# Optimization experiments

Hardware: AMD Instinct MI355X
Metric: run time of the kernel (lower is better)

## Reference

```python
import jax, jax.numpy as jnp
import numpy as np

B, S, H, E, I, MAX_K, A_HID = 2, 2048, 1024, 8, 2688, 6, 50


def setup_inputs() -> dict:
    key = jax.random.key(0)
    ks = jax.random.split(key, 10)
    sc = 0.02
    return {
        "hidden_states": jax.random.normal(ks[0], (B, S, H), dtype=jnp.float32),
        "router_w": jax.random.normal(ks[1], (E, H), dtype=jnp.float32) * sc,
        "actor_w1": jax.random.normal(ks[2], (A_HID, H), dtype=jnp.float32) * sc,
        "actor_b1": jnp.zeros((A_HID,), dtype=jnp.float32),
        "actor_w2": jax.random.normal(ks[3], (MAX_K, A_HID), dtype=jnp.float32) * sc,
        "actor_b2": jnp.zeros((MAX_K,), dtype=jnp.float32),
        "gate_w": jax.random.normal(ks[4], (E, I, H), dtype=jnp.float32) * sc,
        "up_w": jax.random.normal(ks[5], (E, I, H), dtype=jnp.float32) * sc,
        "down_w": jax.random.normal(ks[6], (E, H, I), dtype=jnp.float32) * sc,
    }


def reference(hidden_states, router_w, actor_w1, actor_b1, actor_w2, actor_b2,
              gate_w, up_w, down_w):
    # Router: frozen linear -> softmax probs  [B,S,E]
    probs = jax.nn.softmax(
        jnp.einsum("bsh,eh->bse", hidden_states, router_w).astype(jnp.float32),
        axis=-1)

    # Allocator (ActorCritic.actor): Linear -> GELU -> Linear, clamp(-30,30)
    a_h = jax.nn.gelu(jnp.einsum("bsh,ah->bsa", hidden_states, actor_w1) + actor_b1)
    actor_logits = jnp.clip(
        jnp.einsum("bsa,ka->bsk", a_h, actor_w2) + actor_b2, -30.0, 30.0)
    # deterministic per-token k in [1, MAX_K]
    sampled_k = jnp.argmax(actor_logits, axis=-1) + 1  # [B,S] int

    # dynamic_topk_indices_and_scores: iterative argmax+scatter == select the
    # k highest-prob experts per token; keep their scores, zero elsewhere.
    order = jnp.argsort(-probs, axis=-1)           # descending order of experts
    rank = jnp.argsort(order, axis=-1)             # rank[e] = position of expert e
    mask = rank < sampled_k[..., None]             # [B,S,E] bool, top-k selected
    scores = jnp.where(mask, probs, 0.0).astype(hidden_states.dtype)

    # Expert dispatch-combine: out = sum_e scores[...,e] * LlamaMLP_e(x)
    out = jnp.zeros_like(hidden_states)
    for e in range(E):  # fixed small loop over experts
        g = jnp.einsum("bsh,ih->bsi", hidden_states, gate_w[e])
        u = jnp.einsum("bsh,ih->bsi", hidden_states, up_w[e])
        y = jnp.einsum("bsi,hi->bsh", jax.nn.silu(g) * u, down_w[e])
        out = out + scores[..., e:e + 1] * y
    return out
```

## Files before the change

kernel.cpp:

```cpp
#include <hip/hip_runtime.h>
#include <hip/hip_bf16.h>
#include <stdint.h>

#define TOK 4096
#define HD  1024
#define NE  8
#define ID  2688
#define MAXK 6
#define AHID 50
#define NROW 58
#define KCH 64
#define NCH (HD / KCH)

#define BM 128
#define BN 128
#define BK 64
#define NTM (TOK / BM)
#define NID2 (2 * ID)
#define NTN_GUC (NID2 / BN)
#define NB_GUC (NTN_GUC * NTM)
#define NTN_D (HD / BN)
#define NB_D (NTN_D * NTM)

typedef float  f32x4  __attribute__((ext_vector_type(4)));
typedef __bf16 bf16x8 __attribute__((ext_vector_type(8)));
typedef ushort ushort8v __attribute__((ext_vector_type(8)));

__device__ __forceinline__ ushort f2bf(float f) {
  union { float f; uint32_t u; } v; v.f = f;
  return (ushort)((v.u + 0x7FFFu + ((v.u >> 16) & 1u)) >> 16);
}
__device__ __forceinline__ float bf2f(ushort u) {
  union { uint32_t u; float f; } v; v.u = (uint32_t)u << 16; return v.f;
}

#define GLD_LDS16(gp, lp)                                                      \
  __builtin_amdgcn_global_load_lds(                                            \
      (const __attribute__((address_space(1))) uint32_t*)(uintptr_t)(gp),      \
      (__attribute__((address_space(3))) uint32_t*)(uint32_t)(uintptr_t)(lp),  \
      16, 0, 0)

__global__ void k_cvt(const float* __restrict__ src, ushort* __restrict__ dst, int n) {
  int idx = blockIdx.x * blockDim.x + threadIdx.x;
  int stride = gridDim.x * blockDim.x;
  for (int i = idx * 8; i < n; i += stride * 8) {
    float4 a = *(const float4*)(src + i);
    float4 b = *(const float4*)(src + i + 4);
    ushort8v o;
    o[0] = f2bf(a.x); o[1] = f2bf(a.y); o[2] = f2bf(a.z); o[3] = f2bf(a.w);
    o[4] = f2bf(b.x); o[5] = f2bf(b.y); o[6] = f2bf(b.z); o[7] = f2bf(b.w);
    *(ushort8v*)(dst + i) = o;
  }
}

__global__ void k_cvt_gu(const float* __restrict__ g, const float* __restrict__ u,
                         ushort* __restrict__ dst) {
  const int total = NE * NID2 * (HD / 8);
  int idx = blockIdx.x * blockDim.x + threadIdx.x;
  int stride = gridDim.x * blockDim.x;
  for (int i8 = idx; i8 < total; i8 += stride) {
    const int col = (i8 & (HD / 8 - 1)) * 8;
    const int row = i8 >> 7;
    const int e = row / NID2;
    const int q = row - e * NID2;
    const int p = q >> 7, r = q & 127;
    const float* src = ((r < 64) ? g + ((size_t)e * ID + p * 64 + r) * HD
                                 : u + ((size_t)e * ID + p * 64 + (r - 64)) * HD) + col;
    float4 a = *(const float4*)(src);
    float4 b = *(const float4*)(src + 4);
    ushort8v o;
    o[0] = f2bf(a.x); o[1] = f2bf(a.y); o[2] = f2bf(a.z); o[3] = f2bf(a.w);
    o[4] = f2bf(b.x); o[5] = f2bf(b.y); o[6] = f2bf(b.z); o[7] = f2bf(b.w);
    *(ushort8v*)(dst + (size_t)row * HD + col) = o;
  }
}

__global__ __launch_bounds__(256) void k_logits(
    const float* __restrict__ x, const float* __restrict__ rw,
    const float* __restrict__ aw1, float* __restrict__ partial,
    ushort* __restrict__ Xb) {
  __shared__ float xs[256][KCH + 1];
  const int tid = threadIdx.x;
  const int t0 = blockIdx.x * 256;
  const int c = blockIdx.y;
  const int k0 = c * KCH;
#pragma unroll
  for (int j = 0; j < 16; ++j) {
    const int id4 = j * 256 + tid;
    const int row = id4 >> 4;
    const int c4 = (id4 & 15) * 4;
    float4 v = *(const float4*)(x + (size_t)(t0 + row) * HD + k0 + c4);
    xs[row][c4 + 0] = v.x; xs[row][c4 + 1] = v.y;
    xs[row][c4 + 2] = v.z; xs[row][c4 + 3] = v.w;
    ushort4 o; o.x = f2bf(v.x); o.y = f2bf(v.y); o.z = f2bf(v.z); o.w = f2bf(v.w);
    *(ushort4*)(Xb + (size_t)(t0 + row) * HD + k0 + c4) = o;
  }
  __syncthreads();
  float acc[NROW];
#pragma unroll
  for (int r = 0; r < NROW; ++r) acc[r] = 0.f;
  for (int k4 = 0; k4 < KCH; k4 += 4) {
    const float x0 = xs[tid][k4 + 0], x1 = xs[tid][k4 + 1];
    const float x2 = xs[tid][k4 + 2], x3 = xs[tid][k4 + 3];
#pragma unroll
    for (int r = 0; r < NROW; ++r) {
      const float* wp = ((r < NE) ? (rw + (size_t)r * HD)
                                  : (aw1 + (size_t)(r - NE) * HD)) + k0 + k4;
      acc[r] += x0 * wp[0] + x1 * wp[1] + x2 * wp[2] + x3 * wp[3];
    }
  }
  const int t = t0 + tid;
#pragma unroll
  for (int r = 0; r < NROW; ++r)
    partial[((size_t)c * NROW + r) * TOK + t] = acc[r];
}

__global__ __launch_bounds__(256) void k_reduce(
    const float* __restrict__ partial, float* __restrict__ dots) {
  const int t = blockIdx.x * 256 + threadIdx.x;
  const int r = blockIdx.y;
  float s = 0.f;
#pragma unroll
  for (int c = 0; c < NCH; ++c)
    s += partial[((size_t)c * NROW + r) * TOK + t];
  dots[(size_t)r * TOK + t] = s;
}

__global__ __launch_bounds__(64) void k_select(
    const float* __restrict__ dots, const float* __restrict__ ab1_,
    const float* __restrict__ aw2_, const float* __restrict__ ab2_,
    float* __restrict__ scores, int* __restrict__ idx, int* __restrict__ cnt) {
  const int lane = threadIdx.x;
  const int t = blockIdx.x * 64 + lane;
  float d[NROW];
#pragma unroll
  for (int r = 0; r < NROW; ++r) d[r] = dots[(size_t)r * TOK + t];
  float m = d[0];
#pragma unroll
  for (int e = 1; e < NE; ++e) m = fmaxf(m, d[e]);
  float p[NE]; float sum = 0.f;
#pragma unroll
  for (int e = 0; e < NE; ++e) { p[e] = expf(d[e] - m); sum += p[e]; }
  float inv = 1.f / sum;
#pragma unroll
  for (int e = 0; e < NE; ++e) p[e] *= inv;
  float lg[MAXK];
#pragma unroll
  for (int k = 0; k < MAXK; ++k) lg[k] = ab2_[k];
#pragma unroll
  for (int i = 0; i < AHID; ++i) {
    float v = d[NE + i] + ab1_[i];
    float g = 0.5f * v * (1.f + tanhf(0.7978845608028654f * (v + 0.044715f * v * v * v)));
#pragma unroll
    for (int k = 0; k < MAXK; ++k) lg[k] += g * aw2_[k * AHID + i];
  }
  int best = 0; float bv = fminf(fmaxf(lg[0], -30.f), 30.f);
#pragma unroll
  for (int k = 1; k < MAXK; ++k) {
    float lv = fminf(fmaxf(lg[k], -30.f), 30.f);
    if (lv > bv) { bv = lv; best = k; }
  }
  const int kk = best + 1;
  float sc[NE];
#pragma unroll
  for (int e = 0; e < NE; ++e) {
    int rank = 0;
#pragma unroll
    for (int j = 0; j < NE; ++j)
      rank += (p[j] > p[e]) || (p[j] == p[e] && j < e);
    sc[e] = (rank < kk) ? p[e] : 0.f;
    scores[(size_t)t * NE + e] = sc[e];
  }
#pragma unroll
  for (int e = 0; e < NE; ++e) {
    unsigned long long msk = __ballot(sc[e] > 0.f);
    int npop = __popcll(msk);
    int mypos = __popcll(msk & ((1ull << lane) - 1ull));
    int base = 0;
    if (lane == 0 && npop) base = atomicAdd(cnt + e, npop);
    base = __shfl(base, 0);
    if (sc[e] > 0.f) idx[e * TOK + base + mypos] = t;
  }
}

__global__ __launch_bounds__(256, 2) void k_gateupC(
    const ushort* __restrict__ X, const int* __restrict__ idx,
    const int* __restrict__ cnt, const ushort* __restrict__ Wc,
    ushort* __restrict__ act, const int e0, const int actStrideRows) {
  __shared__ __attribute__((aligned(16))) ushort lds[BM * BK + BN * BK];
  ushort* As = lds;
  ushort* Bs = lds + BM * BK;

  const int e = e0 + blockIdx.z;
  const int n = cnt[e];
  const int bid = blockIdx.x;
  const int logical = (bid & 7) * (NB_GUC / 8) + (bid >> 3);
  const int tn = logical >> 5;
  const int tm = logical & (NTM - 1);
  const int row0 = tm * BM;
  if (row0 >= n) return;
  const int* idx_e = idx + e * TOK;
  const ushort* WcE = Wc + (size_t)e * NID2 * HD;
  ushort* actE = act + (size_t)actStrideRows * e * ID;

  const int tid = threadIdx.x;
  const int lane = tid & 63;
  const int w = tid >> 6;
  const int wr = (w >> 1) * 64;
  const int wc = (w & 1) * 64;
  const int srow = lane >> 3;
  const int scol = (lane & 7) * 8;
  const int col0 = tn * BN;

  f32x4 acc[4][4] = {};

  const ushort* pa[4]; const ushort* pb[4];
  ushort* la[4]; ushort* lb[4];
#pragma unroll
  for (int j = 0; j < 4; ++j) {
    const int cc = w * 4 + j;
    const int r = cc * 8 + srow;
    const int token = idx_e[min(row0 + r, n - 1)];
    pa[j] = X   + (size_t)token * HD + scol;
    pb[j] = WcE + (size_t)(col0 + r) * HD + scol;
    la[j] = &As[cc * 512]; lb[j] = &Bs[cc * 512];
  }

  for (int kt = 0; kt < HD / BK; ++kt) {
    const int k0 = kt * BK;
    __syncthreads();
#pragma unroll
    for (int j = 0; j < 4; ++j) {
      GLD_LDS16(pa[j] + k0, la[j]);
      GLD_LDS16(pb[j] + k0, lb[j]);
    }
    __syncthreads();
#pragma unroll
    for (int kk = 0; kk < 2; ++kk) {
      const int kc = kk * 32 + (lane >> 4) * 8;
      const int rr = lane & 15;
      bf16x8 af[4], bf_[4];
#pragma unroll
      for (int m = 0; m < 4; ++m)
        af[m] = *(const bf16x8*)&As[(wr + m * 16 + rr) * BK + kc];
#pragma unroll
      for (int nn = 0; nn < 4; ++nn)
        bf_[nn] = *(const bf16x8*)&Bs[(wc + nn * 16 + rr) * BK + kc];
#pragma unroll
      for (int m = 0; m < 4; ++m)
#pragma unroll
        for (int nn = 0; nn < 4; ++nn)
          acc[m][nn] = __builtin_amdgcn_mfma_f32_16x16x32_bf16(af[m], bf_[nn], acc[m][nn], 0, 0, 0);
    }
  }

  const int erow = (lane >> 4) * 4, ecol = lane & 15;
  float* exch = (float*)lds;
  __syncthreads();
  if (w & 1) {
#pragma unroll
    for (int m = 0; m < 4; ++m) {
      const int rbase = wr + m * 16 + erow;
#pragma unroll
      for (int nn = 0; nn < 4; ++nn) {
        const int c = nn * 16 + ecol;
#pragma unroll
        for (int j = 0; j < 4; ++j)
          exch[(rbase + j) * 64 + c] = acc[m][nn][j];
      }
    }
  }
  __syncthreads();
  if (!(w & 1)) {
#pragma unroll
    for (int m = 0; m < 4; ++m) {
      const int rbase = wr + m * 16 + erow;
#pragma unroll
      for (int nn = 0; nn < 4; ++nn) {
        const int c = nn * 16 + ecol;
        const int gc = tn * 64 + c;
#pragma unroll
        for (int j = 0; j < 4; ++j) {
          float g = acc[m][nn][j];
          float u = exch[(rbase + j) * 64 + c];
          float h = (g / (1.f + __expf(-g))) * u;
          actE[(size_t)(row0 + rbase + j) * ID + gc] = f2bf(h);
        }
      }
    }
  }
}

__global__ __launch_bounds__(256, 2) void k_down(
    const ushort* __restrict__ act, const ushort* __restrict__ Wd,
    const int* __restrict__ idx, const int* __restrict__ cnt,
    ushort* __restrict__ y) {
  __shared__ __attribute__((aligned(16))) ushort As[BM * BK];
  __shared__ __attribute__((aligned(16))) ushort Bs[BN * BK];

  const int e = blockIdx.z;
  const int n = cnt[e];
  const int bid = blockIdx.x;
  const int logical = (bid & 7) * (NB_D / 8) + (bid >> 3);
  const int tn = logical >> 5;
  const int tm = logical & (NTM - 1);
  const int row0 = tm * BM;
  if (row0 >= n) return;
  const int* idx_e = idx + e * TOK;
  const ushort* A = act + (size_t)e * TOK * ID;
  const ushort* W = Wd + (size_t)e * HD * ID;
  ushort* yE = y + (size_t)e * TOK * HD;

  const int tid = threadIdx.x;
  const int lane = tid & 63;
  const int w = tid >> 6;
  const int wr = (w >> 1) * 64;
  const int wc = (w & 1) * 64;
  const int srow = lane >> 3;
  const int scol = (lane & 7) * 8;
  const int col0 = tn * BN;

  f32x4 acc[4][4] = {};

  const ushort* pa[4]; const ushort* pb[4];
  ushort* la[4]; ushort* lb[4];
#pragma unroll
  for (int j = 0; j < 4; ++j) {
    const int cc = w * 4 + j;
    const int r = cc * 8 + srow;
    pa[j] = A + (size_t)min(row0 + r, n - 1) * ID + scol;
    pb[j] = W + (size_t)(col0 + r) * ID + scol;
    la[j] = &As[cc * 512]; lb[j] = &Bs[cc * 512];
  }

  for (int kt = 0; kt < ID / BK; ++kt) {
    const int k0 = kt * BK;
    __syncthreads();
#pragma unroll
    for (int j = 0; j < 4; ++j) {
      GLD_LDS16(pa[j] + k0, la[j]);
      GLD_LDS16(pb[j] + k0, lb[j]);
    }
    __syncthreads();
#pragma unroll
    for (int kk = 0; kk < 2; ++kk) {
      const int kc = kk * 32 + (lane >> 4) * 8;
      const int rr = lane & 15;
      bf16x8 af[4], bf_[4];
#pragma unroll
      for (int m = 0; m < 4; ++m)
        af[m] = *(const bf16x8*)&As[(wr + m * 16 + rr) * BK + kc];
#pragma unroll
      for (int nn = 0; nn < 4; ++nn)
        bf_[nn] = *(const bf16x8*)&Bs[(wc + nn * 16 + rr) * BK + kc];
#pragma unroll
      for (int m = 0; m < 4; ++m)
#pragma unroll
        for (int nn = 0; nn < 4; ++nn)
          acc[m][nn] = __builtin_amdgcn_mfma_f32_16x16x32_bf16(af[m], bf_[nn], acc[m][nn], 0, 0, 0);
    }
  }

  const int erow = (lane >> 4) * 4, ecol = lane & 15;
#pragma unroll
  for (int m = 0; m < 4; ++m) {
    const int cr0 = row0 + wr + m * 16 + erow;
#pragma unroll
    for (int j = 0; j < 4; ++j) {
      const int cr = cr0 + j;
      if (cr < n) {
        const int token = idx_e[cr];
        ushort* yp = yE + (size_t)token * HD + col0 + wc;
#pragma unroll
        for (int nn = 0; nn < 4; ++nn)
          yp[nn * 16 + ecol] = f2bf(acc[m][nn][j]);
      }
    }
  }
}

__global__ __launch_bounds__(256) void k_combine(
    const ushort* __restrict__ y, const float* __restrict__ scores,
    float* __restrict__ out) {
  const int w = threadIdx.x >> 6, lane = threadIdx.x & 63;
  const int t = blockIdx.x * 4 + w;
  const int c0 = lane * 16;
  float acc[16];
#pragma unroll
  for (int i = 0; i < 16; ++i) acc[i] = 0.f;
  const float* sc = scores + (size_t)t * NE;
#pragma unroll
  for (int e = 0; e < NE; ++e) {
    const float s = sc[e];
    if (s > 0.f) {
      const ushort8v* yp = (const ushort8v*)(y + ((size_t)e * TOK + t) * HD + c0);
      ushort8v v0 = yp[0], v1 = yp[1];
#pragma unroll
      for (int i = 0; i < 8; ++i) acc[i] += s * bf2f(v0[i]);
#pragma unroll
      for (int i = 0; i < 8; ++i) acc[8 + i] += s * bf2f(v1[i]);
    }
  }
  float* op = out + (size_t)t * HD + c0;
#pragma unroll
  for (int i = 0; i < 4; ++i)
    *(float4*)(op + 4 * i) = make_float4(acc[4*i], acc[4*i+1], acc[4*i+2], acc[4*i+3]);
}

__global__ __launch_bounds__(256) void k_down64(
    const ushort* __restrict__ act, const ushort* __restrict__ Wd,
    const float* __restrict__ scores, const int* __restrict__ idx,
    const int* __restrict__ cnt, const int e, float* __restrict__ out) {
  __shared__ __attribute__((aligned(16))) ushort As[64 * 64];
  __shared__ __attribute__((aligned(16))) ushort Bs[64 * 64];
  const int n = cnt[e];
  const int row0 = blockIdx.y * 64;
  if (row0 >= n) return;
  const int* idx_e = idx + e * TOK;
  const ushort* A = act;
  const ushort* W = Wd + (size_t)e * HD * ID;
  const int col0 = blockIdx.x * 64;
  const int tid = threadIdx.x, lane = tid & 63, w = tid >> 6;
  const int wr = (w >> 1) * 32, wc = (w & 1) * 32;
  const int srow = lane >> 3, scol = (lane & 7) * 8;
  f32x4 acc[2][2] = {};
  const ushort* pa[2]; const ushort* pb[2];
  ushort* la[2]; ushort* lb[2];
#pragma unroll
  for (int j = 0; j < 2; ++j) {
    const int cc = w * 2 + j;
    const int r = cc * 8 + srow;
    pa[j] = A + (size_t)min(row0 + r, n - 1) * ID + scol;
    pb[j] = W + (size_t)(col0 + r) * ID + scol;
    la[j] = &As[cc * 512]; lb[j] = &Bs[cc * 512];
  }
  for (int kt = 0; kt < ID / 64; ++kt) {
    const int k0 = kt * 64;
    __syncthreads();
#pragma unroll
    for (int j = 0; j < 2; ++j) { GLD_LDS16(pa[j] + k0, la[j]); GLD_LDS16(pb[j] + k0, lb[j]); }
    __syncthreads();
#pragma unroll
    for (int kk = 0; kk < 2; ++kk) {
      const int kc = kk * 32 + (lane >> 4) * 8;
      const int rr = lane & 15;
      bf16x8 af[2], bf_[2];
#pragma unroll
      for (int m = 0; m < 2; ++m) af[m] = *(const bf16x8*)&As[(wr + m * 16 + rr) * 64 + kc];
#pragma unroll
      for (int nn = 0; nn < 2; ++nn) bf_[nn] = *(const bf16x8*)&Bs[(wc + nn * 16 + rr) * 64 + kc];
#pragma unroll
      for (int m = 0; m < 2; ++m)
#pragma unroll
        for (int nn = 0; nn < 2; ++nn)
          acc[m][nn] = __builtin_amdgcn_mfma_f32_16x16x32_bf16(af[m], bf_[nn], acc[m][nn], 0, 0, 0);
    }
  }
  const int erow = (lane >> 4) * 4, ecol = lane & 15;
#pragma unroll
  for (int m = 0; m < 2; ++m) {
    const int cr0 = row0 + wr + m * 16 + erow;
#pragma unroll
    for (int j = 0; j < 4; ++j) {
      const int cr = cr0 + j;
      if (cr < n) {
        const int token = idx_e[cr];
        const float s = scores[(size_t)token * NE + e];
        float* op = out + (size_t)token * HD + col0 + wc;
#pragma unroll
        for (int nn = 0; nn < 2; ++nn) op[nn * 16 + ecol] += s * acc[m][nn][j];
      }
    }
  }
}

extern "C" void kernel_launch(void* const* d_in, const int* in_sizes, int n_in,
                              void* d_out, int out_size, void* d_ws, size_t ws_size,
                              hipStream_t stream) {
  const float* hs       = (const float*)d_in[0];
  const float* router_w = (const float*)d_in[1];
  const float* actor_w1 = (const float*)d_in[2];
  const float* actor_b1 = (const float*)d_in[3];
  const float* actor_w2 = (const float*)d_in[4];
  const float* actor_b2 = (const float*)d_in[5];
  const float* gate_w   = (const float*)d_in[6];
  const float* up_w     = (const float*)d_in[7];
  const float* down_w   = (const float*)d_in[8];
  float* out = (float*)d_out;

  const size_t sz_x    = (size_t)TOK * HD * 2;
  const size_t sz_w    = (size_t)NE * ID * HD * 2;
  const size_t sz_wgu  = 2 * sz_w;
  const size_t sz_act1 = (size_t)TOK * ID * 2;
  const size_t sz_actC = (size_t)NE * TOK * ID * 2;
  const size_t sz_part = (size_t)NCH * NROW * TOK * 4;
  const size_t sz_dt   = (size_t)NROW * TOK * 4;
  const size_t sz_sc   = (size_t)TOK * NE * 4;
  const size_t sz_ix   = (size_t)NE * TOK * 4;

  const size_t fixed = sz_x + sz_wgu + sz_w;
  const size_t tail  = sz_dt + sz_sc + sz_ix + 256;
  const size_t fb_act = (sz_act1 > sz_part ? sz_act1 : sz_part);
  const size_t need_fb = fixed + fb_act + tail;
  const size_t need_cb = fixed + sz_actC + tail;
  if (ws_size < need_fb) return;
  const bool combined = (ws_size >= need_cb);
  const size_t act_sz = combined ? sz_actC : fb_act;

  char* ws = (char*)d_ws;
  ushort* Xb  = (ushort*)ws;
  ushort* Wgu = (ushort*)(ws + sz_x);
  ushort* Wdb = (ushort*)(ws + sz_x + sz_wgu);
  ushort* yb  = Wgu;
  ushort* act = (ushort*)(ws + fixed);
  float*  partial = (float*)(ws + fixed);
  float*  dots   = (float*)(ws + fixed + act_sz);
  float*  scores = (float*)(ws + fixed + act_sz + sz_dt);
  int*    idx    = (int*)  (ws + fixed + act_sz + sz_dt + sz_sc);
  int*    cnt    = (int*)  (ws + fixed + act_sz + sz_dt + sz_sc + sz_ix);

  hipMemsetAsync(cnt, 0, NE * 4, stream);

  k_cvt_gu<<<2048, 256, 0, stream>>>(gate_w, up_w, Wgu);
  k_cvt<<<2048, 256, 0, stream>>>(down_w, Wdb, NE * ID * HD);

  k_logits<<<dim3(TOK / 256, NCH), 256, 0, stream>>>(hs, router_w, actor_w1, partial, Xb);
  k_reduce<<<dim3(TOK / 256, NROW), 256, 0, stream>>>(partial, dots);
  k_select<<<TOK / 64, 64, 0, stream>>>(dots, actor_b1, actor_w2, actor_b2,
                                        scores, idx, cnt);

  if (combined) {
    k_gateupC<<<dim3(NB_GUC, 1, NE), 256, 0, stream>>>(
        Xb, idx, cnt, Wgu, act, 0, TOK);
    k_down<<<dim3(NB_D, 1, NE), 256, 0, stream>>>(act, Wdb, idx, cnt, yb);
    k_combine<<<TOK / 4, 256, 0, stream>>>(yb, scores, out);
  } else {
    hipMemsetAsync(out, 0, (size_t)TOK * HD * 4, stream);
    for (int e = 0; e < NE; ++e) {
      k_gateupC<<<dim3(NB_GUC, 1, 1), 256, 0, stream>>>(
          Xb, idx, cnt, Wgu, act, e, 0);
      k_down64<<<dim3(HD / 64, TOK / 64), 256, 0, stream>>>(
          act, Wdb, scores, idx, cnt, e, out);
    }
  }
}
```

Measured before the change: 520.8 us.

## Fuse fp32 weight-to-bf16 conversion into expert GEMM tile loads

Drops the separate weight-conversion kernels and has the gate/up and down GEMMs load fp32 weight tiles straight into LDS, converting to bf16 with packed cvt instructions as MFMA operands are formed. This removes a full pass that reads all expert weights and writes bf16 copies before the GEMMs. In exchange each GEMM tile moves twice the weight bytes from global memory and uses more LDS, while the occupancy hint is raised to 3 blocks. The per-expert fallback path and the bf16 weight staging buffers are also removed.

```diff
diff --git a/kernel.cpp b/kernel.cpp
--- a/kernel.cpp
+++ b/kernel.cpp
@@ -33,47 +33,27 @@
 __device__ __forceinline__ float bf2f(ushort u) {
   union { uint32_t u; float f; } v; v.u = (uint32_t)u << 16; return v.f;
 }
+__device__ __forceinline__ uint32_t cvtpk(float lo, float hi) {
+  uint32_t r;
+  asm("v_cvt_pk_bf16_f32 %0, %1, %2" : "=v"(r) : "v"(lo), "v"(hi));
+  return r;
+}
+__device__ __forceinline__ bf16x8 packbf8(const float* bp) {
+  f32x4 b0 = *(const f32x4*)bp;
+  f32x4 b1 = *(const f32x4*)(bp + 4);
+  union { uint32_t u[4]; bf16x8 v; } r;
+  r.u[0] = cvtpk(b0[0], b0[1]);
+  r.u[1] = cvtpk(b0[2], b0[3]);
+  r.u[2] = cvtpk(b1[0], b1[1]);
+  r.u[3] = cvtpk(b1[2], b1[3]);
+  return r.v;
+}
 
 #define GLD_LDS16(gp, lp)                                                      \
   __builtin_amdgcn_global_load_lds(                                            \
       (const __attribute__((address_space(1))) uint32_t*)(uintptr_t)(gp),      \
       (__attribute__((address_space(3))) uint32_t*)(uint32_t)(uintptr_t)(lp),  \
       16, 0, 0)
-
-__global__ void k_cvt(const float* __restrict__ src, ushort* __restrict__ dst, int n) {
-  int idx = blockIdx.x * blockDim.x + threadIdx.x;
-  int stride = gridDim.x * blockDim.x;
-  for (int i = idx * 8; i < n; i += stride * 8) {
-    float4 a = *(const float4*)(src + i);
-    float4 b = *(const float4*)(src + i + 4);
-    ushort8v o;
-    o[0] = f2bf(a.x); o[1] = f2bf(a.y); o[2] = f2bf(a.z); o[3] = f2bf(a.w);
-    o[4] = f2bf(b.x); o[5] = f2bf(b.y); o[6] = f2bf(b.z); o[7] = f2bf(b.w);
-    *(ushort8v*)(dst + i) = o;
-  }
-}
-
-__global__ void k_cvt_gu(const float* __restrict__ g, const float* __restrict__ u,
-                         ushort* __restrict__ dst) {
-  const int total = NE * NID2 * (HD / 8);
-  int idx = blockIdx.x * blockDim.x + threadIdx.x;
-  int stride = gridDim.x * blockDim.x;
-  for (int i8 = idx; i8 < total; i8 += stride) {
-    const int col = (i8 & (HD / 8 - 1)) * 8;
-    const int row = i8 >> 7;
-    const int e = row / NID2;
-    const int q = row - e * NID2;
-    const int p = q >> 7, r = q & 127;
-    const float* src = ((r < 64) ? g + ((size_t)e * ID + p * 64 + r) * HD
-                                 : u + ((size_t)e * ID + p * 64 + (r - 64)) * HD) + col;
-    float4 a = *(const float4*)(src);
-    float4 b = *(const float4*)(src + 4);
-    ushort8v o;
-    o[0] = f2bf(a.x); o[1] = f2bf(a.y); o[2] = f2bf(a.z); o[3] = f2bf(a.w);
-    o[4] = f2bf(b.x); o[5] = f2bf(b.y); o[6] = f2bf(b.z); o[7] = f2bf(b.w);
-    *(ushort8v*)(dst + (size_t)row * HD + col) = o;
-  }
-}
 
 __global__ __launch_bounds__(256) void k_logits(
     const float* __restrict__ x, const float* __restrict__ rw,
@@ -183,15 +163,14 @@
   }
 }
 
-__global__ __launch_bounds__(256, 2) void k_gateupC(
+__global__ __launch_bounds__(256, 3) void k_gateupC(
     const ushort* __restrict__ X, const int* __restrict__ idx,
-    const int* __restrict__ cnt, const ushort* __restrict__ Wc,
-    ushort* __restrict__ act, const int e0, const int actStrideRows) {
-  __shared__ __attribute__((aligned(16))) ushort lds[BM * BK + BN * BK];
-  ushort* As = lds;
-  ushort* Bs = lds + BM * BK;
-
-  const int e = e0 + blockIdx.z;
+    const int* __restrict__ cnt, const float* __restrict__ gw,
+    const float* __restrict__ uw, ushort* __restrict__ act) {
+  __shared__ __attribute__((aligned(16))) ushort As[BM * BK];
+  __shared__ __attribute__((aligned(16))) float  Bs[BN * BK];
+
+  const int e = blockIdx.z;
   const int n = cnt[e];
   const int bid = blockIdx.x;
   const int logical = (bid & 7) * (NB_GUC / 8) + (bid >> 3);
@@ -200,40 +179,47 @@
   const int row0 = tm * BM;
   if (row0 >= n) return;
   const int* idx_e = idx + e * TOK;
-  const ushort* WcE = Wc + (size_t)e * NID2 * HD;
-  ushort* actE = act + (size_t)actStrideRows * e * ID;
-
-  const int tid = threadIdx.x;
-  const int lane = tid & 63;
-  const int w = tid >> 6;
-  const int wr = (w >> 1) * 64;
-  const int wc = (w & 1) * 64;
-  const int srow = lane >> 3;
-  const int scol = (lane & 7) * 8;
-  const int col0 = tn * BN;
+  ushort* actE = act + (size_t)e * TOK * ID;
+
+  const int tid = threadIdx.x, lane = tid & 63, w = tid >> 6;
+  const int wr = (w >> 1) * 64, wc = (w & 1) * 64;
 
   f32x4 acc[4][4] = {};
 
-  const ushort* pa[4]; const ushort* pb[4];
-  ushort* la[4]; ushort* lb[4];
-#pragma unroll
-  for (int j = 0; j < 4; ++j) {
-    const int cc = w * 4 + j;
-    const int r = cc * 8 + srow;
-    const int token = idx_e[min(row0 + r, n - 1)];
-    pa[j] = X   + (size_t)token * HD + scol;
-    pb[j] = WcE + (size_t)(col0 + r) * HD + scol;
-    la[j] = &As[cc * 512]; lb[j] = &Bs[cc * 512];
+  const ushort* pa[4]; ushort* la[4];
+  {
+    const int srow = lane >> 3, scol = (lane & 7) * 8;
+#pragma unroll
+    for (int j = 0; j < 4; ++j) {
+      const int cc = w * 4 + j;
+      const int r = cc * 8 + srow;
+      const int token = idx_e[min(row0 + r, n - 1)];
+      pa[j] = X + (size_t)token * HD + scol;
+      la[j] = &As[cc * 512];
+    }
+  }
+  const float* pb[8]; float* lb[8];
+  {
+    const int srow4 = lane >> 4, scol4 = (lane & 15) * 4;
+#pragma unroll
+    for (int j = 0; j < 8; ++j) {
+      const int g = w * 8 + j;
+      const int rr_ = g * 4 + srow4;
+      const float* base = (rr_ < 64)
+          ? gw + ((size_t)e * ID + tn * 64 + rr_) * HD
+          : uw + ((size_t)e * ID + tn * 64 + (rr_ - 64)) * HD;
+      pb[j] = base + scol4;
+      lb[j] = &Bs[g * 256];
+    }
   }
 
   for (int kt = 0; kt < HD / BK; ++kt) {
     const int k0 = kt * BK;
     __syncthreads();
 #pragma unroll
-    for (int j = 0; j < 4; ++j) {
-      GLD_LDS16(pa[j] + k0, la[j]);
-      GLD_LDS16(pb[j] + k0, lb[j]);
-    }
+    for (int j = 0; j < 4; ++j) GLD_LDS16(pa[j] + k0, la[j]);
+#pragma unroll
+    for (int j = 0; j < 8; ++j) GLD_LDS16(pb[j] + k0, lb[j]);
     __syncthreads();
 #pragma unroll
     for (int kk = 0; kk < 2; ++kk) {
@@ -245,7 +231,7 @@
         af[m] = *(const bf16x8*)&As[(wr + m * 16 + rr) * BK + kc];
 #pragma unroll
       for (int nn = 0; nn < 4; ++nn)
-        bf_[nn] = *(const bf16x8*)&Bs[(wc + nn * 16 + rr) * BK + kc];
+        bf_[nn] = packbf8(&Bs[(wc + nn * 16 + rr) * BK + kc]);
 #pragma unroll
       for (int m = 0; m < 4; ++m)
 #pragma unroll
@@ -255,7 +241,7 @@
   }
 
   const int erow = (lane >> 4) * 4, ecol = lane & 15;
-  float* exch = (float*)lds;
+  float* exch = Bs;
   __syncthreads();
   if (w & 1) {
 #pragma unroll
@@ -291,12 +277,12 @@
   }
 }
 
-__global__ __launch_bounds__(256, 2) void k_down(
-    const ushort* __restrict__ act, const ushort* __restrict__ Wd,
+__global__ __launch_bounds__(256, 3) void k_down(
+    const ushort* __restrict__ act, const float* __restrict__ dw,
     const int* __restrict__ idx, const int* __restrict__ cnt,
     ushort* __restrict__ y) {
   __shared__ __attribute__((aligned(16))) ushort As[BM * BK];
-  __shared__ __attribute__((aligned(16))) ushort Bs[BN * BK];
+  __shared__ __attribute__((aligned(16))) float  Bs[BN * BK];
 
   const int e = blockIdx.z;
   const int n = cnt[e];
@@ -308,39 +294,44 @@
   if (row0 >= n) return;
   const int* idx_e = idx + e * TOK;
   const ushort* A = act + (size_t)e * TOK * ID;
-  const ushort* W = Wd + (size_t)e * HD * ID;
+  const float* dwE = dw + (size_t)e * HD * ID;
   ushort* yE = y + (size_t)e * TOK * HD;
-
-  const int tid = threadIdx.x;
-  const int lane = tid & 63;
-  const int w = tid >> 6;
-  const int wr = (w >> 1) * 64;
-  const int wc = (w & 1) * 64;
-  const int srow = lane >> 3;
-  const int scol = (lane & 7) * 8;
   const int col0 = tn * BN;
 
+  const int tid = threadIdx.x, lane = tid & 63, w = tid >> 6;
+  const int wr = (w >> 1) * 64, wc = (w & 1) * 64;
+
   f32x4 acc[4][4] = {};
 
-  const ushort* pa[4]; const ushort* pb[4];
-  ushort* la[4]; ushort* lb[4];
-#pragma unroll
-  for (int j = 0; j < 4; ++j) {
-    const int cc = w * 4 + j;
-    const int r = cc * 8 + srow;
-    pa[j] = A + (size_t)min(row0 + r, n - 1) * ID + scol;
-    pb[j] = W + (size_t)(col0 + r) * ID + scol;
-    la[j] = &As[cc * 512]; lb[j] = &Bs[cc * 512];
+  const ushort* pa[4]; ushort* la[4];
+  {
+    const int srow = lane >> 3, scol = (lane & 7) * 8;
+#pragma unroll
+    for (int j = 0; j < 4; ++j) {
+      const int cc = w * 4 + j;
+      const int r = cc * 8 + srow;
+      pa[j] = A + (size_t)min(row0 + r, n - 1) * ID + scol;
+      la[j] = &As[cc * 512];
+    }
+  }
+  const float* pb[8]; float* lb[8];
+  {
+    const int srow4 = lane >> 4, scol4 = (lane & 15) * 4;
+#pragma unroll
+    for (int j = 0; j < 8; ++j) {
+      const int g = w * 8 + j;
+      pb[j] = dwE + (size_t)(col0 + g * 4 + srow4) * ID + scol4;
+      lb[j] = &Bs[g * 256];
+    }
   }
 
   for (int kt = 0; kt < ID / BK; ++kt) {
     const int k0 = kt * BK;
     __syncthreads();
 #pragma unroll
-    for (int j = 0; j < 4; ++j) {
-      GLD_LDS16(pa[j] + k0, la[j]);
-      GLD_LDS16(pb[j] + k0, lb[j]);
-    }
+    for (int j = 0; j < 4; ++j) GLD_LDS16(pa[j] + k0, la[j]);
+#pragma unroll
+    for (int j = 0; j < 8; ++j) GLD_LDS16(pb[j] + k0, lb[j]);
     __syncthreads();
 #pragma unroll
     for (int kk = 0; kk < 2; ++kk) {
@@ -352,7 +343,7 @@
         af[m] = *(const bf16x8*)&As[(wr + m * 16 + rr) * BK + kc];
 #pragma unroll
       for (int nn = 0; nn < 4; ++nn)
-        bf_[nn] = *(const bf16x8*)&Bs[(wc + nn * 16 + rr) * BK + kc];
+        bf_[nn] = packbf8(&Bs[(wc + nn * 16 + rr) * BK + kc]);
 #pragma unroll
       for (int m = 0; m < 4; ++m)
 #pragma unroll
@@ -405,73 +396,6 @@
 #pragma unroll
   for (int i = 0; i < 4; ++i)
     *(float4*)(op + 4 * i) = make_float4(acc[4*i], acc[4*i+1], acc[4*i+2], acc[4*i+3]);
-}
-
-__global__ __launch_bounds__(256) void k_down64(
-    const ushort* __restrict__ act, const ushort* __restrict__ Wd,
-    const float* __restrict__ scores, const int* __restrict__ idx,
-    const int* __restrict__ cnt, const int e, float* __restrict__ out) {
-  __shared__ __attribute__((aligned(16))) ushort As[64 * 64];
-  __shared__ __attribute__((aligned(16))) ushort Bs[64 * 64];
-  const int n = cnt[e];
-  const int row0 = blockIdx.y * 64;
-  if (row0 >= n) return;
-  const int* idx_e = idx + e * TOK;
-  const ushort* A = act;
-  const ushort* W = Wd + (size_t)e * HD * ID;
-  const int col0 = blockIdx.x * 64;
-  const int tid = threadIdx.x, lane = tid & 63, w = tid >> 6;
-  const int wr = (w >> 1) * 32, wc = (w & 1) * 32;
-  const int srow = lane >> 3, scol = (lane & 7) * 8;
-  f32x4 acc[2][2] = {};
-  const ushort* pa[2]; const ushort* pb[2];
-  ushort* la[2]; ushort* lb[2];
-#pragma unroll
-  for (int j = 0; j < 2; ++j) {
-    const int cc = w * 2 + j;
-    const int r = cc * 8 + srow;
-    pa[j] = A + (size_t)min(row0 + r, n - 1) * ID + scol;
-    pb[j] = W + (size_t)(col0 + r) * ID + scol;
-    la[j] = &As[cc * 512]; lb[j] = &Bs[cc * 512];
-  }
-  for (int kt = 0; kt < ID / 64; ++kt) {
-    const int k0 = kt * 64;
-    __syncthreads();
-#pragma unroll
-    for (int j = 0; j < 2; ++j) { GLD_LDS16(pa[j] + k0, la[j]); GLD_LDS16(pb[j] + k0, lb[j]); }
-    __syncthreads();
-#pragma unroll
-    for (int kk = 0; kk < 2; ++kk) {
-      const int kc = kk * 32 + (lane >> 4) * 8;
-      const int rr = lane & 15;
-      bf16x8 af[2], bf_[2];
-#pragma unroll
-      for (int m = 0; m < 2; ++m) af[m] = *(const bf16x8*)&As[(wr + m * 16 + rr) * 64 + kc];
-#pragma unroll
-      for (int nn = 0; nn < 2; ++nn) bf_[nn] = *(const bf16x8*)&Bs[(wc + nn * 16 + rr) * 64 + kc];
-#pragma unroll
-      for (int m = 0; m < 2; ++m)
-#pragma unroll
-        for (int nn = 0; nn < 2; ++nn)
-          acc[m][nn] = __builtin_amdgcn_mfma_f32_16x16x32_bf16(af[m], bf_[nn], acc[m][nn], 0, 0, 0);
-    }
-  }
-  const int erow = (lane >> 4) * 4, ecol = lane & 15;
-#pragma unroll
-  for (int m = 0; m < 2; ++m) {
-    const int cr0 = row0 + wr + m * 16 + erow;
-#pragma unroll
-    for (int j = 0; j < 4; ++j) {
-      const int cr = cr0 + j;
-      if (cr < n) {
-        const int token = idx_e[cr];
-        const float s = scores[(size_t)token * NE + e];
-        float* op = out + (size_t)token * HD + col0 + wc;
-#pragma unroll
-        for (int nn = 0; nn < 2; ++nn) op[nn * 16 + ecol] += s * acc[m][nn][j];
-      }
-    }
-  }
 }
 
 extern "C" void kernel_launch(void* const* d_in, const int* in_sizes, int n_in,
@@ -488,59 +412,42 @@
   const float* down_w   = (const float*)d_in[8];
   float* out = (float*)d_out;
 
-  const size_t sz_x    = (size_t)TOK * HD * 2;
-  const size_t sz_w    = (size_t)NE * ID * HD * 2;
-  const size_t sz_wgu  = 2 * sz_w;
-  const size_t sz_act1 = (size_t)TOK * ID * 2;
-  const size_t sz_actC = (size_t)NE * TOK * ID * 2;
+  const size_t sz_xb  = (size_t)TOK * HD * 2;
+  const size_t sz_act = (size_t)NE * TOK * ID * 2;
+  const size_t sz_y   = (size_t)NE * TOK * HD * 2;
   const size_t sz_part = (size_t)NCH * NROW * TOK * 4;
-  const size_t sz_dt   = (size_t)NROW * TOK * 4;
-  const size_t sz_sc   = (size_t)TOK * NE * 4;
-  const size_t sz_ix   = (size_t)NE * TOK * 4;
-
-  const size_t fixed = sz_x + sz_wgu + sz_w;
-  const size_t tail  = sz_dt + sz_sc + sz_ix + 256;
-  const size_t fb_act = (sz_act1 > sz_part ? sz_act1 : sz_part);
-  const size_t need_fb = fixed + fb_act + tail;
-  const size_t need_cb = fixed + sz_actC + tail;
-  if (ws_size < need_fb) return;
-  const bool combined = (ws_size >= need_cb);
-  const size_t act_sz = combined ? sz_actC : fb_act;
+  const size_t sz_dt  = (size_t)NROW * TOK * 4;
+  const size_t sz_sc  = (size_t)TOK * NE * 4;
+  const size_t sz_ix  = (size_t)NE * TOK * 4;
+
+  const size_t ofs_act = sz_xb;
+  const size_t ofs_y   = ofs_act + sz_act;
+  const size_t ofs_dt  = ofs_y + (sz_y > sz_part ? sz_y : sz_part);
+  const size_t ofs_sc  = ofs_dt + sz_dt;
+  const size_t ofs_ix  = ofs_sc + sz_sc;
+  const size_t ofs_cnt = ofs_ix + sz_ix;
+  const size_t need = ofs_cnt + 256;
+  if (ws_size < need) return;
 
   char* ws = (char*)d_ws;
-  ushort* Xb  = (ushort*)ws;
-  ushort* Wgu = (ushort*)(ws + sz_x);
-  ushort* Wdb = (ushort*)(ws + sz_x + sz_wgu);
-  ushort* yb  = Wgu;
-  ushort* act = (ushort*)(ws + fixed);
-  float*  partial = (float*)(ws + fixed);
-  float*  dots   = (float*)(ws + fixed + act_sz);
-  float*  scores = (float*)(ws + fixed + act_sz + sz_dt);
-  int*    idx    = (int*)  (ws + fixed + act_sz + sz_dt + sz_sc);
-  int*    cnt    = (int*)  (ws + fixed + act_sz + sz_dt + sz_sc + sz_ix);
+  ushort* Xb      = (ushort*)ws;
+  ushort* act     = (ushort*)(ws + ofs_act);
+  ushort* yb      = (ushort*)(ws + ofs_y);
+  float*  partial = (float*) (ws + ofs_y);
+  float*  dots    = (float*) (ws + ofs_dt);
+  float*  scores  = (float*) (ws + ofs_sc);
+  int*    idx     = (int*)   (ws + ofs_ix);
+  int*    cnt     = (int*)   (ws + ofs_cnt);
 
   hipMemsetAsync(cnt, 0, NE * 4, stream);
-
-  k_cvt_gu<<<2048, 256, 0, stream>>>(gate_w, up_w, Wgu);
-  k_cvt<<<2048, 256, 0, stream>>>(down_w, Wdb, NE * ID * HD);
 
   k_logits<<<dim3(TOK / 256, NCH), 256, 0, stream>>>(hs, router_w, actor_w1, partial, Xb);
   k_reduce<<<dim3(TOK / 256, NROW), 256, 0, stream>>>(partial, dots);
   k_select<<<TOK / 64, 64, 0, stream>>>(dots, actor_b1, actor_w2, actor_b2,
                                         scores, idx, cnt);
 
-  if (combined) {
-    k_gateupC<<<dim3(NB_GUC, 1, NE), 256, 0, stream>>>(
-        Xb, idx, cnt, Wgu, act, 0, TOK);
-    k_down<<<dim3(NB_D, 1, NE), 256, 0, stream>>>(act, Wdb, idx, cnt, yb);
-    k_combine<<<TOK / 4, 256, 0, stream>>>(yb, scores, out);
-  } else {
-    hipMemsetAsync(out, 0, (size_t)TOK * HD * 4, stream);
-    for (int e = 0; e < NE; ++e) {
-      k_gateupC<<<dim3(NB_GUC, 1, 1), 256, 0, stream>>>(
-          Xb, idx, cnt, Wgu, act, e, 0);
-      k_down64<<<dim3(HD / 64, TOK / 64), 256, 0, stream>>>(
-          act, Wdb, scores, idx, cnt, e, out);
-    }
-  }
-}
+  k_gateupC<<<dim3(NB_GUC, 1, NE), 256, 0, stream>>>(
+      Xb, idx, cnt, gate_w, up_w, act);
+  k_down<<<dim3(NB_D, 1, NE), 256, 0, stream>>>(act, down_w, idx, cnt, yb);
+  k_combine<<<TOK / 4, 256, 0, stream>>>(yb, scores, out);
+}
```

Measured after the change: 864.2 us. 65.9% more time.
